# Kernel tuning notes

Measured on AMD Instinct MI355X. Metric: run time of the kernel, lower is better.

## Reference

```python
import jax, jax.numpy as jnp
import numpy as np

B, FEAT, SPD_H, CTRL_H, N_CMD = 32768, 512, 128, 256, 4


def _p(key, shape, fan_in):
    # torch nn.Linear default init: U(-1/sqrt(fan_in), 1/sqrt(fan_in))
    lim = 1.0 / np.sqrt(fan_in)
    return jax.random.uniform(key, shape, jnp.float32, -lim, lim)


def setup_inputs() -> dict:
    key = jax.random.key(0)
    ks = iter(jax.random.split(key, 32))
    inp = {
        "feat": jax.random.normal(next(ks), (B, FEAT), jnp.float32),
        "speed": jax.random.uniform(next(ks), (B,), jnp.float32),
        "command": jax.random.randint(next(ks), (B,), 0, N_CMD, jnp.int32),
        "ms_w1": _p(next(ks), (1, SPD_H), 1), "ms_b1": _p(next(ks), (SPD_H,), 1),
        "ms_w2": _p(next(ks), (SPD_H, SPD_H), SPD_H), "ms_b2": _p(next(ks), (SPD_H,), SPD_H),
        "ms_w3": _p(next(ks), (SPD_H, SPD_H), SPD_H), "ms_b3": _p(next(ks), (SPD_H,), SPD_H),
        # speed_pred_module: 512 -> 256 -> 256 -> 1
        "sp_w1": _p(next(ks), (FEAT, CTRL_H), FEAT), "sp_b1": _p(next(ks), (CTRL_H,), FEAT),
        "sp_w2": _p(next(ks), (CTRL_H, CTRL_H), CTRL_H), "sp_b2": _p(next(ks), (CTRL_H,), CTRL_H),
        "sp_w3": _p(next(ks), (CTRL_H, 1), CTRL_H), "sp_b3": _p(next(ks), (1,), CTRL_H),
        # join_module: Linear(640, 512)
        "join_w": _p(next(ks), (FEAT + SPD_H, FEAT), FEAT + SPD_H),
        "join_b": _p(next(ks), (FEAT,), FEAT + SPD_H),
        # 4 control heads: 512 -> 256 -> 256 -> 3 (stacked on expert axis e)
        "ctrl_w1": _p(next(ks), (N_CMD, FEAT, CTRL_H), FEAT), "ctrl_b1": _p(next(ks), (N_CMD, CTRL_H), FEAT),
        "ctrl_w2": _p(next(ks), (N_CMD, CTRL_H, CTRL_H), CTRL_H), "ctrl_b2": _p(next(ks), (N_CMD, CTRL_H), CTRL_H),
        "ctrl_w3": _p(next(ks), (N_CMD, CTRL_H, 3), CTRL_H), "ctrl_b3": _p(next(ks), (N_CMD, 3), CTRL_H),
    }
    return inp


def _mlp(x, w1, b1, w2, b2, w3, b3):
    # FullyConnectedNet: Linear, ReLU, Linear, Dropout(p=0 -> noop), ReLU, Linear
    h = jax.nn.relu(x @ w1 + b1)
    h = jax.nn.relu(h @ w2 + b2)
    return h @ w3 + b3


def reference(feat, speed, command,
              ms_w1, ms_b1, ms_w2, ms_b2, ms_w3, ms_b3,
              sp_w1, sp_b1, sp_w2, sp_b2, sp_w3, sp_b3,
              join_w, join_b,
              ctrl_w1, ctrl_b1, ctrl_w2, ctrl_b2, ctrl_w3, ctrl_b3):
    v = _mlp(speed[:, None], ms_w1, ms_b1, ms_w2, ms_b2, ms_w3, ms_b3)      # [B,128]
    joined = jnp.concatenate([feat, v], axis=1) @ join_w + join_b           # [B,512]
    v_p = _mlp(feat, sp_w1, sp_b1, sp_w2, sp_b2, sp_w3, sp_b3)              # [B,1]
    # command-indexed dispatch: compute all 4 heads densely, then select per sample
    h1 = jax.nn.relu(jnp.einsum('bd,edh->beh', joined, ctrl_w1) + ctrl_b1)  # [B,4,256]
    h2 = jax.nn.relu(jnp.einsum('beh,ehk->bek', h1, ctrl_w2) + ctrl_b2)     # [B,4,256]
    act_all = jnp.einsum('bek,eko->beo', h2, ctrl_w3) + ctrl_b3             # [B,4,3]
    action = jnp.take_along_axis(act_all, command[:, None, None].astype(jnp.int32), axis=1)[:, 0]  # [B,3]
    throttle = jax.nn.sigmoid(action[:, 0])
    steering = jnp.tanh(action[:, 1])
    brake = jax.nn.sigmoid(action[:, 2])
    return v_p, throttle, brake, steering
```

## Files before the change

kernel.cpp:

```cpp
#include <hip/hip_runtime.h>
#include <hip/hip_bf16.h>
#include <stdint.h>
#include <math.h>

#define BB 32768
#define FEAT 512
#define SPD_H 128
#define CTRL_H 256
#define NCMD 4

typedef __attribute__((ext_vector_type(8))) short bf16x8;
typedef __attribute__((ext_vector_type(4))) float f32x4;

__device__ __forceinline__ unsigned short f2bf(float f) {
  union { float f; uint32_t u; } v; v.f = f;
  uint32_t u = v.u;
  return (unsigned short)((u + 0x7fffu + ((u >> 16) & 1u)) >> 16);
}

__device__ __forceinline__ void async16(const unsigned short* g, unsigned short* l) {
  __builtin_amdgcn_global_load_lds(
      (const __attribute__((address_space(1))) unsigned int*)g,
      (__attribute__((address_space(3))) unsigned int*)l, 16, 0, 0);
}

struct WSeg { const float* src; unsigned short* dst; int K; int N; int ldd; };
struct PrepArgs {
  WSeg s[12];
  int start[13];
  const float* join_w; unsigned short* wjbf;
  const float* feat; unsigned short* ajoin;
  const int* cmd; int* wavecnt;
};
__global__ void k_prep(PrepArgs a) {
  int bx = blockIdx.x, t = threadIdx.x;
  if (bx < 16384) {
    int idx = bx * 256 + t;
    int i = idx >> 7;
    int j4 = (idx & 127) << 2;
    float4 f = *(const float4*)(a.feat + (size_t)i * FEAT + j4);
    ushort4 o;
    o.x = f2bf(f.x); o.y = f2bf(f.y); o.z = f2bf(f.z); o.w = f2bf(f.w);
    *(ushort4*)(a.ajoin + (size_t)i * 640 + j4) = o;
    return;
  }
  int rel = bx - 16384;
  if (rel < 320) {
    int idx = rel * 256 + t;
    float4 f = *(const float4*)(a.join_w + (size_t)idx * 4);
    ushort4 o;
    o.x = f2bf(f.x); o.y = f2bf(f.y); o.z = f2bf(f.z); o.w = f2bf(f.w);
    *(ushort4*)(a.wjbf + (size_t)idx * 4) = o;
    return;
  }
  rel -= 320;
  if (rel < a.start[12]) {
    int si = 0;
    while (rel >= a.start[si + 1]) ++si;
    WSeg sg = a.s[si];
    int tile = rel - a.start[si];
    int tkx = sg.K >> 5;
    int tn = tile / tkx;
    int tk = tile - tn * tkx;
    int k0 = tk * 32, n0 = tn * 32;
    __shared__ float tb[32][33];
    int tx = t & 31, ty = t >> 5;
#pragma unroll
    for (int j = 0; j < 4; ++j)
      tb[ty + j * 8][tx] = sg.src[(size_t)(k0 + ty + j * 8) * sg.N + n0 + tx];
    __syncthreads();
#pragma unroll
    for (int j = 0; j < 4; ++j)
      sg.dst[(size_t)(n0 + ty + j * 8) * sg.ldd + k0 + tx] = f2bf(tb[tx][ty + j * 8]);
    return;
  }
  rel -= a.start[12];
  int i = rel * 256 + t;
  int c = a.cmd[i];
  int wid = i >> 6;
  int lane = t & 63;
#pragma unroll
  for (int cv = 0; cv < NCMD; ++cv) {
    unsigned long long m = __ballot(c == cv);
    if (lane == 0) a.wavecnt[cv * 512 + wid] = __popcll(m);
  }
}

__launch_bounds__(256)
__global__ void k_ms(const float* __restrict__ speed,
                     const float* __restrict__ w1, const float* __restrict__ b1,
                     const unsigned short* __restrict__ w2t, const float* __restrict__ b2,
                     const unsigned short* __restrict__ w3t, const float* __restrict__ b3,
                     unsigned short* __restrict__ ajoin) {
  __shared__ unsigned short hw[128][136];
  __shared__ unsigned short Bs[128 * 32];
  const int m0 = blockIdx.x * 128;
  const int t = threadIdx.x;
  const int w = t >> 6, lane = t & 63;
  const int wm = w & 1, wn = w >> 1;
  const int fr = lane & 15, fk = (lane >> 4) * 8;
  const int rquad = (lane >> 4) * 4, cidx = lane & 15;

  {
    int r = t >> 1, half = t & 1;
    float s = speed[m0 + r];
#pragma unroll
    for (int c0 = 0; c0 < 64; c0 += 4) {
      int c = half * 64 + c0;
      float4 wv = *(const float4*)(w1 + c);
      float4 bv = *(const float4*)(b1 + c);
      hw[r][c + 0] = f2bf(fmaxf(fmaf(s, wv.x, bv.x), 0.f));
      hw[r][c + 1] = f2bf(fmaxf(fmaf(s, wv.y, bv.y), 0.f));
      hw[r][c + 2] = f2bf(fmaxf(fmaf(s, wv.z, bv.z), 0.f));
      hw[r][c + 3] = f2bf(fmaxf(fmaf(s, wv.w, bv.w), 0.f));
    }
  }
  __syncthreads();

  for (int layer = 0; layer < 2; ++layer) {
    const unsigned short* Wt = layer ? w3t : w2t;
    const float* bb = layer ? b3 : b2;
    f32x4 acc[4][4];
#pragma unroll
    for (int i = 0; i < 4; ++i)
#pragma unroll
      for (int j = 0; j < 4; ++j)
#pragma unroll
        for (int r = 0; r < 4; ++r) acc[i][j][r] = 0.f;

    for (int k0 = 0; k0 < 128; k0 += 32) {
#pragma unroll
      for (int it = 0; it < 2; ++it) {
        int row = w * 32 + it * 16 + (lane >> 2);
        async16(Wt + (size_t)row * 128 + k0 + (lane & 3) * 8,
                Bs + (w * 32 + it * 16) * 32);
      }
      __syncthreads();
      bf16x8 af[4], bfv[4];
#pragma unroll
      for (int i = 0; i < 4; ++i)
        af[i] = *(const bf16x8*)(&hw[wm * 64 + i * 16 + fr][k0 + fk]);
#pragma unroll
      for (int j = 0; j < 4; ++j)
        bfv[j] = *(const bf16x8*)(Bs + (wn * 64 + j * 16 + fr) * 32 + fk);
#pragma unroll
      for (int i = 0; i < 4; ++i)
#pragma unroll
        for (int j = 0; j < 4; ++j)
          acc[i][j] = __builtin_amdgcn_mfma_f32_16x16x32_bf16(af[i], bfv[j], acc[i][j], 0, 0, 0);
      __syncthreads();
    }
#pragma unroll
    for (int j = 0; j < 4; ++j) {
      int col = wn * 64 + j * 16 + cidx;
      float bv = bb[col];
#pragma unroll
      for (int i = 0; i < 4; ++i) {
        int row = wm * 64 + i * 16 + rquad;
#pragma unroll
        for (int r = 0; r < 4; ++r) {
          float v = acc[i][j][r] + bv;
          if (layer == 0) v = fmaxf(v, 0.f);
          hw[row + r][col] = f2bf(v);
        }
      }
    }
    __syncthreads();
  }
  {
    int r = t >> 1, half = t & 1;
#pragma unroll
    for (int c8 = 0; c8 < 8; ++c8)
      *(bf16x8*)(ajoin + (size_t)(m0 + r) * 640 + 512 + half * 64 + c8 * 8) =
          *(const bf16x8*)(&hw[r][half * 64 + c8 * 8]);
  }
}

__launch_bounds__(256)
__global__ void k_gemm(const unsigned short* __restrict__ A, int lda,
                       const int* __restrict__ perm,
                       const int* __restrict__ seg,
                       const unsigned short* __restrict__ Wt, int wstride,
                       const float* __restrict__ bias, int bstride,
                       unsigned short* __restrict__ C, int ldc,
                       int relu_flag, int M, int K) {
  __shared__ unsigned short As[128 * 32];
  __shared__ unsigned short Bs[128 * 32];
  __shared__ float fscr[32][132];

  const int gid = blockIdx.x;
  const int mt = gid & 255;
  const int nt = gid >> 8;
  const int e = blockIdx.z;
  int m_start = 0, m_cnt = M;
  if (seg) { m_start = seg[e]; m_cnt = seg[e + 1] - m_start; }
  const int m0 = mt * 128;
  if (m0 >= m_cnt) return;
  const int n0 = nt * 128;
  const unsigned short* W = Wt + (size_t)e * wstride;
  const float* bi = bias ? (bias + (size_t)e * bstride) : nullptr;

  const int t = threadIdx.x;
  const int w = t >> 6, lane = t & 63;
  const int wm = w & 1, wn = w >> 1;

  f32x4 acc[4][4];
#pragma unroll
  for (int i = 0; i < 4; ++i)
#pragma unroll
    for (int j = 0; j < 4; ++j)
#pragma unroll
      for (int r = 0; r < 4; ++r) acc[i][j][r] = 0.f;

  const int fr = lane & 15;
  const int fk = (lane >> 4) * 8;

  const unsigned short* agp[2]; const unsigned short* bgp[2];
  unsigned short* al[2]; unsigned short* bl[2];
#pragma unroll
  for (int it = 0; it < 2; ++it) {
    int row = w * 32 + it * 16 + (lane >> 2);
    int seg8 = (lane & 3) * 8;
    int rl = m0 + row;
    if (rl >= m_cnt) rl = m_cnt - 1;
    int grow = perm ? perm[m_start + rl] : (m_start + rl);
    agp[it] = A + (size_t)grow * lda + seg8;
    bgp[it] = W + (size_t)(n0 + row) * K + seg8;
    al[it] = As + (w * 32 + it * 16) * 32;
    bl[it] = Bs + (w * 32 + it * 16) * 32;
  }

  for (int k0 = 0; k0 < K; k0 += 32) {
#pragma unroll
    for (int it = 0; it < 2; ++it) {
      async16(agp[it] + k0, al[it]);
      async16(bgp[it] + k0, bl[it]);
    }
    __syncthreads();
    bf16x8 af[4], bfv[4];
#pragma unroll
    for (int i = 0; i < 4; ++i)
      af[i] = *(const bf16x8*)(As + (wm * 64 + i * 16 + fr) * 32 + fk);
#pragma unroll
    for (int j = 0; j < 4; ++j)
      bfv[j] = *(const bf16x8*)(Bs + (wn * 64 + j * 16 + fr) * 32 + fk);
#pragma unroll
    for (int i = 0; i < 4; ++i)
#pragma unroll
      for (int j = 0; j < 4; ++j)
        acc[i][j] = __builtin_amdgcn_mfma_f32_16x16x32_bf16(af[i], bfv[j], acc[i][j], 0, 0, 0);
    __syncthreads();
  }

  const int rquad = (lane >> 4) * 4;
  const int cidx = lane & 15;
  const bool rel = (relu_flag != 0);

  float bv[4];
#pragma unroll
  for (int j = 0; j < 4; ++j) bv[j] = bi ? bi[n0 + wn * 64 + j * 16 + cidx] : 0.f;

#pragma unroll
  for (int c = 0; c < 4; ++c) {
    if (wm == (c >> 1)) {
#pragma unroll
      for (int j = 0; j < 4; ++j) {
#pragma unroll
        for (int ii = 0; ii < 2; ++ii) {
          int i = 2 * (c & 1) + ii;
          int lr = ii * 16 + rquad;
#pragma unroll
          for (int r = 0; r < 4; ++r) {
            float v = acc[i][j][r] + bv[j];
            if (rel) v = fmaxf(v, 0.f);
            fscr[lr + r][wn * 64 + j * 16 + cidx] = v;
          }
        }
      }
    }
    __syncthreads();
#pragma unroll
    for (int q = 0; q < 2; ++q) {
      int sg = t + 256 * q;
      int lr = sg >> 4, cs = (sg & 15) * 8;
      int grow = m0 + c * 32 + lr;
      if (grow < m_cnt) {
        union { bf16x8 v; unsigned short u[8]; } pk;
#pragma unroll
        for (int x = 0; x < 8; ++x) pk.u[x] = f2bf(fscr[lr][cs + x]);
        *(bf16x8*)(C + (size_t)(m_start + grow) * ldc + (n0 + cs)) = pk.v;
      }
    }
    __syncthreads();
  }
}

struct VArgs {
  const unsigned short* A_s; const unsigned short* A_c;
  const unsigned short* W_s; const unsigned short* W_c;
  const float* b_s; const float* b_c;
  const float* w3_s; const float* b3_s;
  const float* w3_c; const float* b3_c;
  const int* perm; const int* seg;
  float* out;
};
__launch_bounds__(256)
__global__ void k_vgemm(VArgs a) {
  __shared__ unsigned short As[64 * 32];
  __shared__ unsigned short Bs[256 * 32];
  const int z = blockIdx.z;
  const unsigned short* A; const unsigned short* W; const float* bi;
  int m_start, m_cnt;
  if (z == 4) { A = a.A_s; W = a.W_s; bi = a.b_s; m_start = 0; m_cnt = BB; }
  else {
    A = a.A_c; W = a.W_c + (size_t)z * 65536; bi = a.b_c + z * 256;
    m_start = a.seg[z]; m_cnt = a.seg[z + 1] - m_start;
  }
  const int m0 = blockIdx.x * 64;
  if (m0 >= m_cnt) return;
  const int t = threadIdx.x, w = t >> 6, lane = t & 63;
  const int fr = lane & 15, fk = (lane >> 4) * 8;

  f32x4 acc[16];
#pragma unroll
  for (int j = 0; j < 16; ++j)
#pragma unroll
    for (int r = 0; r < 4; ++r) acc[j][r] = 0.f;

  int arow = m0 + w * 16 + (lane >> 2);
  if (arow >= m_cnt) arow = m_cnt - 1;
  const unsigned short* ap = A + (size_t)(m_start + arow) * 256 + (lane & 3) * 8;
  unsigned short* al = As + (w * 16) * 32;
  const unsigned short* bp[4]; unsigned short* bl[4];
#pragma unroll
  for (int it = 0; it < 4; ++it) {
    int brow = w * 64 + it * 16 + (lane >> 2);
    bp[it] = W + (size_t)brow * 256 + (lane & 3) * 8;
    bl[it] = Bs + (w * 64 + it * 16) * 32;
  }

  for (int k0 = 0; k0 < 256; k0 += 32) {
    async16(ap + k0, al);
#pragma unroll
    for (int it = 0; it < 4; ++it) async16(bp[it] + k0, bl[it]);
    __syncthreads();
    bf16x8 af = *(const bf16x8*)(As + (w * 16 + fr) * 32 + fk);
#pragma unroll
    for (int j = 0; j < 16; ++j) {
      bf16x8 bfv = *(const bf16x8*)(Bs + (j * 16 + fr) * 32 + fk);
      acc[j] = __builtin_amdgcn_mfma_f32_16x16x32_bf16(af, bfv, acc[j], 0, 0, 0);
    }
    __syncthreads();
  }

  const int rquad = (lane >> 4) * 4;
  float bcol[16];
#pragma unroll
  for (int j = 0; j < 16; ++j) bcol[j] = bi[j * 16 + fr];

  if (z == 4) {
    float aw[16];
#pragma unroll
    for (int j = 0; j < 16; ++j) aw[j] = a.w3_s[j * 16 + fr];
#pragma unroll
    for (int r = 0; r < 4; ++r) {
      float s = 0.f;
#pragma unroll
      for (int j = 0; j < 16; ++j)
        s = fmaf(fmaxf(acc[j][r] + bcol[j], 0.f), aw[j], s);
      s += __shfl_xor(s, 1, 64);
      s += __shfl_xor(s, 2, 64);
      s += __shfl_xor(s, 4, 64);
      s += __shfl_xor(s, 8, 64);
      int row = m0 + w * 16 + rquad + r;
      if (fr == 0 && row < m_cnt) a.out[row] = s + a.b3_s[0];
    }
  } else {
    float aw0[16], aw1[16], aw2[16];
#pragma unroll
    for (int j = 0; j < 16; ++j) {
      const float* wp = a.w3_c + (size_t)z * 768 + (j * 16 + fr) * 3;
      aw0[j] = wp[0]; aw1[j] = wp[1]; aw2[j] = wp[2];
    }
#pragma unroll
    for (int r = 0; r < 4; ++r) {
      float s0 = 0.f, s1 = 0.f, s2 = 0.f;
#pragma unroll
      for (int j = 0; j < 16; ++j) {
        float v = fmaxf(acc[j][r] + bcol[j], 0.f);
        s0 = fmaf(v, aw0[j], s0);
        s1 = fmaf(v, aw1[j], s1);
        s2 = fmaf(v, aw2[j], s2);
      }
#pragma unroll
      for (int m = 1; m <= 8; m <<= 1) {
        s0 += __shfl_xor(s0, m, 64);
        s1 += __shfl_xor(s1, m, 64);
        s2 += __shfl_xor(s2, m, 64);
      }
      int row = m0 + w * 16 + rquad + r;
      if (fr == 0 && row < m_cnt) {
        int orig = a.perm[m_start + row];
        float a0 = s0 + a.b3_c[z * 3 + 0];
        float a1 = s1 + a.b3_c[z * 3 + 1];
        float a2 = s2 + a.b3_c[z * 3 + 2];
        a.out[BB + orig]     = 1.f / (1.f + __expf(-a0));
        a.out[2 * BB + orig] = 1.f / (1.f + __expf(-a2));
        a.out[3 * BB + orig] = tanhf(a1);
      }
    }
  }
}

__global__ void k_place(const int* __restrict__ cmd, const int* __restrict__ wavecnt,
                        int* __restrict__ perm, int* __restrict__ offs,
                        const float* __restrict__ join_b,
                        const float* __restrict__ ctrl_w1,
                        const float* __restrict__ ctrl_b1,
                        float* __restrict__ b_f) {
  int b = blockIdx.x, t = threadIdx.x;
  if (b >= 128) {
    int e = b - 128;
    float s = ctrl_b1[e * 256 + t];
    const float* w = ctrl_w1 + (size_t)e * 512 * 256 + t;
    for (int m = 0; m < 512; ++m) s = fmaf(join_b[m], w[(size_t)m * 256], s);
    b_f[e * 256 + t] = s;
    return;
  }
  __shared__ int pf[NCMD][4];
  __shared__ int tot[NCMD];
  int c = t >> 6, lane = t & 63;
  int v[8]; int s = 0;
#pragma unroll
  for (int q = 0; q < 8; ++q) { v[q] = wavecnt[c * 512 + lane * 8 + q]; s += v[q]; }
  int p = s;
#pragma unroll
  for (int m = 1; m < 64; m <<= 1) { int o = __shfl_up(p, m, 64); if (lane >= m) p += o; }
  int excl = p - s;
  if (lane == 63) tot[c] = p;
  if (lane == ((4 * b) >> 3)) {
    int base_off = (4 * b) & 7;
    int run = excl;
#pragma unroll
    for (int q = 0; q < 8; ++q) {
      if (q >= base_off && q < base_off + 4) pf[c][q - base_off] = run;
      run += v[q];
    }
  }
  __syncthreads();
  int soffs[NCMD + 1];
  soffs[0] = 0;
#pragma unroll
  for (int e = 0; e < NCMD; ++e) soffs[e + 1] = soffs[e] + tot[e];
  if (b == 0 && t == 0)
    for (int e = 0; e <= NCMD; ++e) offs[e] = soffs[e];
  int i = b * 256 + t;
  int mc = cmd[i];
  int lwid = t >> 6;
  int rank = 0, base = 0;
#pragma unroll
  for (int cv = 0; cv < NCMD; ++cv) {
    unsigned long long m = __ballot(mc == cv);
    if (mc == cv) {
      rank = __popcll(m & ((1ull << lane) - 1ull));
      base = soffs[cv] + pf[cv][lwid];
    }
  }
  perm[base + rank] = i;
}

static inline size_t align256(size_t x) { return (x + 255) & ~(size_t)255; }

extern "C" void kernel_launch(void* const* d_in, const int* in_sizes, int n_in,
                              void* d_out, int out_size, void* d_ws, size_t ws_size,
                              hipStream_t stream) {
  const float* feat   = (const float*)d_in[0];
  const float* speed  = (const float*)d_in[1];
  const int*   command= (const int*)d_in[2];
  const float* ms_w1  = (const float*)d_in[3];
  const float* ms_b1  = (const float*)d_in[4];
  const float* ms_w2  = (const float*)d_in[5];
  const float* ms_b2  = (const float*)d_in[6];
  const float* ms_w3  = (const float*)d_in[7];
  const float* ms_b3  = (const float*)d_in[8];
  const float* sp_w1  = (const float*)d_in[9];
  const float* sp_b1  = (const float*)d_in[10];
  const float* sp_w2  = (const float*)d_in[11];
  const float* sp_b2  = (const float*)d_in[12];
  const float* sp_w3  = (const float*)d_in[13];
  const float* sp_b3  = (const float*)d_in[14];
  const float* join_w = (const float*)d_in[15];
  const float* join_b = (const float*)d_in[16];
  const float* ctrl_w1= (const float*)d_in[17];
  const float* ctrl_b1= (const float*)d_in[18];
  const float* ctrl_w2= (const float*)d_in[19];
  const float* ctrl_b2= (const float*)d_in[20];
  const float* ctrl_w3= (const float*)d_in[21];
  const float* ctrl_b3= (const float*)d_in[22];
  float* out = (float*)d_out;

  char* ws = (char*)d_ws;
  size_t off = 0;
  auto alloc = [&](size_t bytes) -> char* { char* p = ws + off; off = align256(off + bytes); return p; };

  unsigned short* ajoin  = (unsigned short*)alloc((size_t)BB * 640 * 2);
  unsigned short* sph1   = (unsigned short*)alloc((size_t)BB * 256 * 2);
  unsigned short* ch1    = (unsigned short*)alloc((size_t)BB * 256 * 2);
  unsigned short* wtp    = (unsigned short*)alloc(1998848ull * 2);
  int* perm    = (int*)alloc((size_t)BB * 4);
  int* cnt     = (int*)alloc(64);
  int* wavecnt = (int*)alloc(4 * 512 * 4);
  float* b_f   = (float*)alloc(4 * 256 * 4);

  unsigned short* sp_w1t = wtp;
  unsigned short* sp_w2t = wtp + 131072;
  unsigned short* ms_w2t = wtp + 196608;
  unsigned short* ms_w3t = wtp + 212992;
  unsigned short* c_w1t  = wtp + 229376;
  unsigned short* c_w2t  = wtp + 753664;
  unsigned short* wjbf   = wtp + 1015808;
  unsigned short* wf_t   = wtp + 1343488;

  PrepArgs P;
  P.s[0] = { sp_w1, sp_w1t, 512, 256, 512 };
  P.s[1] = { sp_w2, sp_w2t, 256, 256, 256 };
  P.s[2] = { ms_w2, ms_w2t, 128, 128, 128 };
  P.s[3] = { ms_w3, ms_w3t, 128, 128, 128 };
  for (int e = 0; e < 4; ++e) P.s[4 + e] = { ctrl_w1 + (size_t)e * 512 * 256, c_w1t + (size_t)e * 131072, 512, 256, 512 };
  for (int e = 0; e < 4; ++e) P.s[8 + e] = { ctrl_w2 + (size_t)e * 256 * 256, c_w2t + (size_t)e * 65536, 256, 256, 256 };
  P.start[0] = 0;
  for (int i = 0; i < 12; ++i)
    P.start[i + 1] = P.start[i] + (P.s[i].K >> 5) * (P.s[i].N >> 5);
  P.join_w = join_w; P.wjbf = wjbf;
  P.feat = feat; P.ajoin = ajoin;
  P.cmd = command; P.wavecnt = wavecnt;
  int prep_blocks = 16384 + 320 + P.start[12] + 128;

  k_prep<<<prep_blocks, 256, 0, stream>>>(P);
  k_ms<<<256, 256, 0, stream>>>(speed, ms_w1, ms_b1, ms_w2t, ms_b2, ms_w3t, ms_b3, ajoin);
  k_place<<<132, 256, 0, stream>>>(command, wavecnt, perm, cnt + 4,
                                   join_b, ctrl_w1, ctrl_b1, b_f);

  k_gemm<<<5 * 256, 256, 0, stream>>>(c_w1t, 512, nullptr, nullptr,
      wjbf, 0, nullptr, 0, wf_t, 640, 0, 1024, 512);

  k_gemm<<<2 * 256, 256, 0, stream>>>(ajoin, 640, nullptr, nullptr,
      sp_w1t, 0, sp_b1, 0, sph1, 256, 1, BB, 512);

  k_gemm<<<dim3(2 * 256, 1, 4), 256, 0, stream>>>(ajoin, 640, perm, cnt + 4,
      wf_t, 256 * 640, b_f, 256, ch1, 256, 1, BB, 640);

  VArgs V;
  V.A_s = sph1; V.A_c = ch1; V.W_s = sp_w2t; V.W_c = c_w2t;
  V.b_s = sp_b2; V.b_c = ctrl_b2;
  V.w3_s = sp_w3; V.b3_s = sp_b3; V.w3_c = ctrl_w3; V.b3_c = ctrl_b3;
  V.perm = perm; V.seg = cnt + 4; V.out = out;
  k_vgemm<<<dim3(512, 1, 5), 256, 0, stream>>>(V);
}
```

Baseline: 267.7 us.

## Merge small launches: fold bias fold into prep, fuse place+weight GEMM, batch layer-1 GEMMs

Moves the folded bias computation into the prep kernel, combines the permutation placement with the weight-folding GEMM in one kernel, and launches the speed-pred layer-1 GEMM together with the four expert layer-1 GEMMs as one grid (z=5). The goal is fewer kernel launches and less tail idle time between dependent small kernels. It also removes the separate k_gemm in favour of a shared device function. The slow serial bias loop now sits in the large prep grid, which could lengthen its tail.

```diff
diff --git a/kernel.cpp b/kernel.cpp
--- a/kernel.cpp
+++ b/kernel.cpp
@@ -22,6 +22,112 @@
   __builtin_amdgcn_global_load_lds(
       (const __attribute__((address_space(1))) unsigned int*)g,
       (__attribute__((address_space(3))) unsigned int*)l, 16, 0, 0);
+}
+
+__device__ __forceinline__ void gemm128(
+    const unsigned short* __restrict__ A, int lda,
+    const int* __restrict__ perm, int m_start, int m_cnt,
+    const unsigned short* __restrict__ W, const float* __restrict__ bi,
+    unsigned short* __restrict__ C, int ldc, int relu, int K, int mt, int nt) {
+  __shared__ unsigned short As[128 * 32];
+  __shared__ unsigned short Bs[128 * 32];
+  __shared__ float fscr[32][132];
+
+  const int m0 = mt * 128;
+  if (m0 >= m_cnt) return;
+  const int n0 = nt * 128;
+  const int t = threadIdx.x;
+  const int w = t >> 6, lane = t & 63;
+  const int wm = w & 1, wn = w >> 1;
+
+  f32x4 acc[4][4];
+#pragma unroll
+  for (int i = 0; i < 4; ++i)
+#pragma unroll
+    for (int j = 0; j < 4; ++j)
+#pragma unroll
+      for (int r = 0; r < 4; ++r) acc[i][j][r] = 0.f;
+
+  const int fr = lane & 15;
+  const int fk = (lane >> 4) * 8;
+
+  const unsigned short* agp[2]; const unsigned short* bgp[2];
+  unsigned short* al[2]; unsigned short* bl[2];
+#pragma unroll
+  for (int it = 0; it < 2; ++it) {
+    int row = w * 32 + it * 16 + (lane >> 2);
+    int seg8 = (lane & 3) * 8;
+    int rl = m0 + row;
+    if (rl >= m_cnt) rl = m_cnt - 1;
+    int grow = perm ? perm[m_start + rl] : (m_start + rl);
+    agp[it] = A + (size_t)grow * lda + seg8;
+    bgp[it] = W + (size_t)(n0 + row) * K + seg8;
+    al[it] = As + (w * 32 + it * 16) * 32;
+    bl[it] = Bs + (w * 32 + it * 16) * 32;
+  }
+
+  for (int k0 = 0; k0 < K; k0 += 32) {
+#pragma unroll
+    for (int it = 0; it < 2; ++it) {
+      async16(agp[it] + k0, al[it]);
+      async16(bgp[it] + k0, bl[it]);
+    }
+    __syncthreads();
+    bf16x8 af[4], bfv[4];
+#pragma unroll
+    for (int i = 0; i < 4; ++i)
+      af[i] = *(const bf16x8*)(As + (wm * 64 + i * 16 + fr) * 32 + fk);
+#pragma unroll
+    for (int j = 0; j < 4; ++j)
+      bfv[j] = *(const bf16x8*)(Bs + (wn * 64 + j * 16 + fr) * 32 + fk);
+#pragma unroll
+    for (int i = 0; i < 4; ++i)
+#pragma unroll
+      for (int j = 0; j < 4; ++j)
+        acc[i][j] = __builtin_amdgcn_mfma_f32_16x16x32_bf16(af[i], bfv[j], acc[i][j], 0, 0, 0);
+    __syncthreads();
+  }
+
+  const int rquad = (lane >> 4) * 4;
+  const int cidx = lane & 15;
+
+  float bv[4];
+#pragma unroll
+  for (int j = 0; j < 4; ++j) bv[j] = bi ? bi[n0 + wn * 64 + j * 16 + cidx] : 0.f;
+
+#pragma unroll
+  for (int c = 0; c < 4; ++c) {
+    if (wm == (c >> 1)) {
+#pragma unroll
+      for (int j = 0; j < 4; ++j) {
+#pragma unroll
+        for (int ii = 0; ii < 2; ++ii) {
+          int i = 2 * (c & 1) + ii;
+          int lr = ii * 16 + rquad;
+#pragma unroll
+          for (int r = 0; r < 4; ++r) {
+            float v = acc[i][j][r] + bv[j];
+            if (relu) v = fmaxf(v, 0.f);
+            fscr[lr + r][wn * 64 + j * 16 + cidx] = v;
+          }
+        }
+      }
+    }
+    __syncthreads();
+#pragma unroll
+    for (int q = 0; q < 2; ++q) {
+      int sg = t + 256 * q;
+      int lr = sg >> 4, cs = (sg & 15) * 8;
+      int grow = m0 + c * 32 + lr;
+      if (grow < m_cnt) {
+        union { bf16x8 v; unsigned short u[8]; } pk;
+#pragma unroll
+        for (int x = 0; x < 8; ++x) pk.u[x] = f2bf(fscr[lr][cs + x]);
+        *(bf16x8*)(C + (size_t)(m_start + grow) * ldc + (n0 + cs)) = pk.v;
+      }
+    }
+    __syncthreads();
+  }
 }
 
 struct WSeg { const float* src; unsigned short* dst; int K; int N; int ldd; };
@@ -31,6 +137,7 @@
   const float* join_w; unsigned short* wjbf;
   const float* feat; unsigned short* ajoin;
   const int* cmd; int* wavecnt;
+  const float* join_b; const float* ctrl_w1; const float* ctrl_b1; float* b_f;
 };
 __global__ void k_prep(PrepArgs a) {
   int bx = blockIdx.x, t = threadIdx.x;
@@ -75,15 +182,23 @@
     return;
   }
   rel -= a.start[12];
-  int i = rel * 256 + t;
-  int c = a.cmd[i];
-  int wid = i >> 6;
-  int lane = t & 63;
-#pragma unroll
-  for (int cv = 0; cv < NCMD; ++cv) {
-    unsigned long long m = __ballot(c == cv);
-    if (lane == 0) a.wavecnt[cv * 512 + wid] = __popcll(m);
-  }
+  if (rel < 128) {
+    int i = rel * 256 + t;
+    int c = a.cmd[i];
+    int wid = i >> 6;
+    int lane = t & 63;
+#pragma unroll
+    for (int cv = 0; cv < NCMD; ++cv) {
+      unsigned long long m = __ballot(c == cv);
+      if (lane == 0) a.wavecnt[cv * 512 + wid] = __popcll(m);
+    }
+    return;
+  }
+  int e = rel - 128;
+  float s = a.ctrl_b1[e * 256 + t];
+  const float* w = a.ctrl_w1 + (size_t)e * 512 * 256 + t;
+  for (int m = 0; m < 512; ++m) s = fmaf(a.join_b[m], w[(size_t)m * 256], s);
+  a.b_f[e * 256 + t] = s;
 }
 
 __launch_bounds__(256)
@@ -176,122 +291,79 @@
   }
 }
 
+struct MidArgs {
+  const int* cmd; const int* wavecnt; int* perm; int* offs;
+  const unsigned short* c_w1t; const unsigned short* wjbf; unsigned short* wf_t;
+};
 __launch_bounds__(256)
-__global__ void k_gemm(const unsigned short* __restrict__ A, int lda,
-                       const int* __restrict__ perm,
-                       const int* __restrict__ seg,
-                       const unsigned short* __restrict__ Wt, int wstride,
-                       const float* __restrict__ bias, int bstride,
-                       unsigned short* __restrict__ C, int ldc,
-                       int relu_flag, int M, int K) {
-  __shared__ unsigned short As[128 * 32];
-  __shared__ unsigned short Bs[128 * 32];
-  __shared__ float fscr[32][132];
-
+__global__ void k_mid(MidArgs a) {
+  int b = blockIdx.x, t = threadIdx.x;
+  if (b >= 128) {
+    int idx = b - 128;
+    int mt = idx & 7, nt = idx >> 3;
+    gemm128(a.c_w1t, 512, nullptr, 0, 1024, a.wjbf, nullptr, a.wf_t, 640, 0, 512, mt, nt);
+    return;
+  }
+  __shared__ int pf[NCMD][4];
+  __shared__ int tot[NCMD];
+  int c = t >> 6, lane = t & 63;
+  int v[8]; int s = 0;
+#pragma unroll
+  for (int q = 0; q < 8; ++q) { v[q] = a.wavecnt[c * 512 + lane * 8 + q]; s += v[q]; }
+  int p = s;
+#pragma unroll
+  for (int m = 1; m < 64; m <<= 1) { int o = __shfl_up(p, m, 64); if (lane >= m) p += o; }
+  int excl = p - s;
+  if (lane == 63) tot[c] = p;
+  if (lane == ((4 * b) >> 3)) {
+    int base_off = (4 * b) & 7;
+    int run = excl;
+#pragma unroll
+    for (int q = 0; q < 8; ++q) {
+      if (q >= base_off && q < base_off + 4) pf[c][q - base_off] = run;
+      run += v[q];
+    }
+  }
+  __syncthreads();
+  int soffs[NCMD + 1];
+  soffs[0] = 0;
+#pragma unroll
+  for (int e = 0; e < NCMD; ++e) soffs[e + 1] = soffs[e] + tot[e];
+  if (b == 0 && t == 0)
+    for (int e = 0; e <= NCMD; ++e) a.offs[e] = soffs[e];
+  int i = b * 256 + t;
+  int mc = a.cmd[i];
+  int lwid = t >> 6;
+  int rank = 0, base = 0;
+#pragma unroll
+  for (int cv = 0; cv < NCMD; ++cv) {
+    unsigned long long m = __ballot(mc == cv);
+    if (mc == cv) {
+      rank = __popcll(m & ((1ull << lane) - 1ull));
+      base = soffs[cv] + pf[cv][lwid];
+    }
+  }
+  a.perm[base + rank] = i;
+}
+
+struct MainArgs {
+  const unsigned short* ajoin;
+  const unsigned short* wf_t; const float* b_f;
+  const unsigned short* sp_w1t; const float* sp_b1;
+  unsigned short* ch1; unsigned short* sph1;
+  const int* perm; const int* seg;
+};
+__launch_bounds__(256)
+__global__ void k_main(MainArgs a) {
+  const int z = blockIdx.z;
   const int gid = blockIdx.x;
-  const int mt = gid & 255;
-  const int nt = gid >> 8;
-  const int e = blockIdx.z;
-  int m_start = 0, m_cnt = M;
-  if (seg) { m_start = seg[e]; m_cnt = seg[e + 1] - m_start; }
-  const int m0 = mt * 128;
-  if (m0 >= m_cnt) return;
-  const int n0 = nt * 128;
-  const unsigned short* W = Wt + (size_t)e * wstride;
-  const float* bi = bias ? (bias + (size_t)e * bstride) : nullptr;
-
-  const int t = threadIdx.x;
-  const int w = t >> 6, lane = t & 63;
-  const int wm = w & 1, wn = w >> 1;
-
-  f32x4 acc[4][4];
-#pragma unroll
-  for (int i = 0; i < 4; ++i)
-#pragma unroll
-    for (int j = 0; j < 4; ++j)
-#pragma unroll
-      for (int r = 0; r < 4; ++r) acc[i][j][r] = 0.f;
-
-  const int fr = lane & 15;
-  const int fk = (lane >> 4) * 8;
-
-  const unsigned short* agp[2]; const unsigned short* bgp[2];
-  unsigned short* al[2]; unsigned short* bl[2];
-#pragma unroll
-  for (int it = 0; it < 2; ++it) {
-    int row = w * 32 + it * 16 + (lane >> 2);
-    int seg8 = (lane & 3) * 8;
-    int rl = m0 + row;
-    if (rl >= m_cnt) rl = m_cnt - 1;
-    int grow = perm ? perm[m_start + rl] : (m_start + rl);
-    agp[it] = A + (size_t)grow * lda + seg8;
-    bgp[it] = W + (size_t)(n0 + row) * K + seg8;
-    al[it] = As + (w * 32 + it * 16) * 32;
-    bl[it] = Bs + (w * 32 + it * 16) * 32;
-  }
-
-  for (int k0 = 0; k0 < K; k0 += 32) {
-#pragma unroll
-    for (int it = 0; it < 2; ++it) {
-      async16(agp[it] + k0, al[it]);
-      async16(bgp[it] + k0, bl[it]);
-    }
-    __syncthreads();
-    bf16x8 af[4], bfv[4];
-#pragma unroll
-    for (int i = 0; i < 4; ++i)
-      af[i] = *(const bf16x8*)(As + (wm * 64 + i * 16 + fr) * 32 + fk);
-#pragma unroll
-    for (int j = 0; j < 4; ++j)
-      bfv[j] = *(const bf16x8*)(Bs + (wn * 64 + j * 16 + fr) * 32 + fk);
-#pragma unroll
-    for (int i = 0; i < 4; ++i)
-#pragma unroll
-      for (int j = 0; j < 4; ++j)
-        acc[i][j] = __builtin_amdgcn_mfma_f32_16x16x32_bf16(af[i], bfv[j], acc[i][j], 0, 0, 0);
-    __syncthreads();
-  }
-
-  const int rquad = (lane >> 4) * 4;
-  const int cidx = lane & 15;
-  const bool rel = (relu_flag != 0);
-
-  float bv[4];
-#pragma unroll
-  for (int j = 0; j < 4; ++j) bv[j] = bi ? bi[n0 + wn * 64 + j * 16 + cidx] : 0.f;
-
-#pragma unroll
-  for (int c = 0; c < 4; ++c) {
-    if (wm == (c >> 1)) {
-#pragma unroll
-      for (int j = 0; j < 4; ++j) {
-#pragma unroll
-        for (int ii = 0; ii < 2; ++ii) {
-          int i = 2 * (c & 1) + ii;
-          int lr = ii * 16 + rquad;
-#pragma unroll
-          for (int r = 0; r < 4; ++r) {
-            float v = acc[i][j][r] + bv[j];
-            if (rel) v = fmaxf(v, 0.f);
-            fscr[lr + r][wn * 64 + j * 16 + cidx] = v;
-          }
-        }
-      }
-    }
-    __syncthreads();
-#pragma unroll
-    for (int q = 0; q < 2; ++q) {
-      int sg = t + 256 * q;
-      int lr = sg >> 4, cs = (sg & 15) * 8;
-      int grow = m0 + c * 32 + lr;
-      if (grow < m_cnt) {
-        union { bf16x8 v; unsigned short u[8]; } pk;
-#pragma unroll
-        for (int x = 0; x < 8; ++x) pk.u[x] = f2bf(fscr[lr][cs + x]);
-        *(bf16x8*)(C + (size_t)(m_start + grow) * ldc + (n0 + cs)) = pk.v;
-      }
-    }
-    __syncthreads();
+  const int mt = gid & 255, nt = gid >> 8;
+  if (z == 4) {
+    gemm128(a.ajoin, 640, nullptr, 0, BB, a.sp_w1t, a.sp_b1, a.sph1, 256, 1, 512, mt, nt);
+  } else {
+    int ms = a.seg[z], mc = a.seg[z + 1] - ms;
+    gemm128(a.ajoin, 640, a.perm, ms, mc, a.wf_t + (size_t)z * 256 * 640,
+            a.b_f + z * 256, a.ch1, 256, 1, 640, mt, nt);
   }
 }
 
@@ -410,63 +482,6 @@
       }
     }
   }
-}
-
-__global__ void k_place(const int* __restrict__ cmd, const int* __restrict__ wavecnt,
-                        int* __restrict__ perm, int* __restrict__ offs,
-                        const float* __restrict__ join_b,
-                        const float* __restrict__ ctrl_w1,
-                        const float* __restrict__ ctrl_b1,
-                        float* __restrict__ b_f) {
-  int b = blockIdx.x, t = threadIdx.x;
-  if (b >= 128) {
-    int e = b - 128;
-    float s = ctrl_b1[e * 256 + t];
-    const float* w = ctrl_w1 + (size_t)e * 512 * 256 + t;
-    for (int m = 0; m < 512; ++m) s = fmaf(join_b[m], w[(size_t)m * 256], s);
-    b_f[e * 256 + t] = s;
-    return;
-  }
-  __shared__ int pf[NCMD][4];
-  __shared__ int tot[NCMD];
-  int c = t >> 6, lane = t & 63;
-  int v[8]; int s = 0;
-#pragma unroll
-  for (int q = 0; q < 8; ++q) { v[q] = wavecnt[c * 512 + lane * 8 + q]; s += v[q]; }
-  int p = s;
-#pragma unroll
-  for (int m = 1; m < 64; m <<= 1) { int o = __shfl_up(p, m, 64); if (lane >= m) p += o; }
-  int excl = p - s;
-  if (lane == 63) tot[c] = p;
-  if (lane == ((4 * b) >> 3)) {
-    int base_off = (4 * b) & 7;
-    int run = excl;
-#pragma unroll
-    for (int q = 0; q < 8; ++q) {
-      if (q >= base_off && q < base_off + 4) pf[c][q - base_off] = run;
-      run += v[q];
-    }
-  }
-  __syncthreads();
-  int soffs[NCMD + 1];
-  soffs[0] = 0;
-#pragma unroll
-  for (int e = 0; e < NCMD; ++e) soffs[e + 1] = soffs[e] + tot[e];
-  if (b == 0 && t == 0)
-    for (int e = 0; e <= NCMD; ++e) offs[e] = soffs[e];
-  int i = b * 256 + t;
-  int mc = cmd[i];
-  int lwid = t >> 6;
-  int rank = 0, base = 0;
-#pragma unroll
-  for (int cv = 0; cv < NCMD; ++cv) {
-    unsigned long long m = __ballot(mc == cv);
-    if (mc == cv) {
-      rank = __popcll(m & ((1ull << lane) - 1ull));
-      base = soffs[cv] + pf[cv][lwid];
-    }
-  }
-  perm[base + rank] = i;
 }
 
 static inline size_t align256(size_t x) { return (x + 255) & ~(size_t)255; }
@@ -534,21 +549,23 @@
   P.join_w = join_w; P.wjbf = wjbf;
   P.feat = feat; P.ajoin = ajoin;
   P.cmd = command; P.wavecnt = wavecnt;
-  int prep_blocks = 16384 + 320 + P.start[12] + 128;
+  P.join_b = join_b; P.ctrl_w1 = ctrl_w1; P.ctrl_b1 = ctrl_b1; P.b_f = b_f;
+  int prep_blocks = 16384 + 320 + P.start[12] + 128 + 4;
 
   k_prep<<<prep_blocks, 256, 0, stream>>>(P);
   k_ms<<<256, 256, 0, stream>>>(speed, ms_w1, ms_b1, ms_w2t, ms_b2, ms_w3t, ms_b3, ajoin);
-  k_place<<<132, 256, 0, stream>>>(command, wavecnt, perm, cnt + 4,
-                                   join_b, ctrl_w1, ctrl_b1, b_f);
-
-  k_gemm<<<5 * 256, 256, 0, stream>>>(c_w1t, 512, nullptr, nullptr,
-      wjbf, 0, nullptr, 0, wf_t, 640, 0, 1024, 512);
-
-  k_gemm<<<2 * 256, 256, 0, stream>>>(ajoin, 640, nullptr, nullptr,
-      sp_w1t, 0, sp_b1, 0, sph1, 256, 1, BB, 512);
-
-  k_gemm<<<dim3(2 * 256, 1, 4), 256, 0, stream>>>(ajoin, 640, perm, cnt + 4,
-      wf_t, 256 * 640, b_f, 256, ch1, 256, 1, BB, 640);
+
+  MidArgs Mi;
+  Mi.cmd = command; Mi.wavecnt = wavecnt; Mi.perm = perm; Mi.offs = cnt + 4;
+  Mi.c_w1t = c_w1t; Mi.wjbf = wjbf; Mi.wf_t = wf_t;
+  k_mid<<<168, 256, 0, stream>>>(Mi);
+
+  MainArgs Ma;
+  Ma.ajoin = ajoin; Ma.wf_t = wf_t; Ma.b_f = b_f;
+  Ma.sp_w1t = sp_w1t; Ma.sp_b1 = sp_b1;
+  Ma.ch1 = ch1; Ma.sph1 = sph1;
+  Ma.perm = perm; Ma.seg = cnt + 4;
+  k_main<<<dim3(512, 1, 5), 256, 0, stream>>>(Ma);
 
   VArgs V;
   V.A_s = sph1; V.A_c = ch1; V.W_s = sp_w2t; V.W_c = c_w2t;
```

Measured after the change: 248.2 us. -7.3%, faster.
